# Kernel tuning notes

Hardware: AMD Instinct MI355X
Metric: run time of the kernel (lower is better)

Reference implementation:

```python
import jax, jax.numpy as jnp
import numpy as np

N_KNOTS = 8
LATENT = 16
DEGREE = 3


def _de_boor(x, t, c, p):
    # x: arbitrary-shape query points; t: (n_knots+6,) padded knots; c: (n_knots+2,) control points
    k = jnp.digitize(x, t) - 1  # interval index per element (binary search gather)
    d = [c[k + (j - p)] for j in range(p + 1)]
    for r in range(1, p + 1):
        for j in range(p, r - 1, -1):
            t_lo = t[k + (j - p)]
            t_hi = t[k + (j + 1 - r)]
            alpha = (x - t_lo) / (t_hi - t_lo)
            d[j] = (1.0 - alpha) * d[j - 1] + alpha * d[j]
    return d[p]


def setup_inputs() -> dict:
    key = jax.random.key(0)
    ks = jax.random.split(key, 8)
    # |k| grid normalized to fftfreq range: values in [0, sqrt(3)]
    x = jax.random.uniform(ks[0], (256, 256, 256), dtype=jnp.float32) * 1.7320508
    a = jax.random.uniform(ks[1], (1,), dtype=jnp.float32)  # scale factor in (0,1)
    inv = 1.0 / np.sqrt(LATENT).astype(np.float32)
    W1 = jax.random.normal(ks[2], (1, LATENT), jnp.float32)
    b1 = jnp.zeros((LATENT,), jnp.float32)
    W2 = jax.random.normal(ks[3], (LATENT, LATENT), jnp.float32) * inv
    b2 = jnp.zeros((LATENT,), jnp.float32)
    Ww = jax.random.normal(ks[4], (LATENT, N_KNOTS + 1), jnp.float32) * inv
    bw = jnp.zeros((N_KNOTS + 1,), jnp.float32)
    Wk = jax.random.normal(ks[5], (LATENT, N_KNOTS - 1), jnp.float32) * inv
    bk = jnp.zeros((N_KNOTS - 1,), jnp.float32)
    return {"x": x, "a": a, "W1": W1, "b1": b1, "W2": W2, "b2": b2,
            "Ww": Ww, "bw": bw, "Wk": Wk, "bk": bk}


def reference(x, a, W1, b1, W2, b2, Ww, bw, Wk, bk):
    # tiny MLP on scalar a -> spline weights w and knot increments k
    net = jnp.sin(a @ W1 + b1)           # (LATENT,)
    net = jnp.sin(net @ W2 + b2)         # (LATENT,)
    w = net @ Ww + bw                    # (N_KNOTS+1,)
    kk = net @ Wk + bk                   # (N_KNOTS-1,)
    kk = jnp.concatenate([jnp.zeros((1,), x.dtype), jnp.cumsum(jax.nn.softmax(kk))])  # (N_KNOTS,), monotone in [0,1]
    w = jnp.concatenate([jnp.zeros((1,), x.dtype), w])                                 # (N_KNOTS+2,)
    ak = jnp.concatenate([jnp.zeros((3,), x.dtype), kk, jnp.ones((3,), x.dtype)])      # padded knots
    xq = jnp.clip(x / jnp.sqrt(jnp.asarray(3.0, x.dtype)), 0.0, 1.0 - 0.0001)
    return _de_boor(xq, ak, w, DEGREE)
```

## Files before the change

### kernel.cpp

```cpp
#include <hip/hip_runtime.h>
#include <math.h>

typedef float f4 __attribute__((ext_vector_type(4)));

__device__ __forceinline__ float eval_one(float xv,
                                          float c0, float c1, float c2, float c3,
                                          float k1, float k2, float k3,
                                          float k4, float k5, float k6,
                                          float e1, float e2, float e3,
                                          float e4, float e5, float e6)
{
    const float xq = fminf(fmaxf(xv * 0.57735026918962576f, 0.0f), 0.9999f);
    float acc = fmaf(fmaf(fmaf(c3, xq, c2), xq, c1), xq, c0);
    float r;
    r = fmaxf(xq - k1, 0.f); acc = fmaf(e1 * r, r * r, acc);
    r = fmaxf(xq - k2, 0.f); acc = fmaf(e2 * r, r * r, acc);
    r = fmaxf(xq - k3, 0.f); acc = fmaf(e3 * r, r * r, acc);
    r = fmaxf(xq - k4, 0.f); acc = fmaf(e4 * r, r * r, acc);
    r = fmaxf(xq - k5, 0.f); acc = fmaf(e5 * r, r * r, acc);
    r = fmaxf(xq - k6, 0.f); acc = fmaf(e6 * r, r * r, acc);
    return acc;
}

__global__ __launch_bounds__(256) void nsf_fused_kernel(
    const float* __restrict__ x,
    const float* __restrict__ a,
    const float* __restrict__ W1, const float* __restrict__ b1,
    const float* __restrict__ W2, const float* __restrict__ b2,
    const float* __restrict__ Ww, const float* __restrict__ bw,
    const float* __restrict__ Wk, const float* __restrict__ bk,
    float* __restrict__ out, int n)
{
    const int n4 = n >> 2;
    const int gid = blockIdx.x * blockDim.x + threadIdx.x;
    const int stride = gridDim.x * blockDim.x;
    const f4* __restrict__ x4 = reinterpret_cast<const f4*>(x);
    f4* __restrict__ o4 = reinterpret_cast<f4*>(out);

    f4 v[8];
#pragma unroll
    for (int it = 0; it < 8; ++it) {
        const int idx = gid + it * stride;
        if (idx < n4) v[it] = __builtin_nontemporal_load(x4 + idx);
    }

    const int lane = threadIdx.x & 63;
    const int j16 = lane & 15;

    const float n1own = __sinf(a[0] * W1[j16] + b1[j16]);
    float s2 = b2[j16];
#pragma unroll
    for (int i = 0; i < 16; ++i)
        s2 = fmaf(__shfl(n1own, i, 64), W2[i * 16 + j16], s2);
    const float n2own = __sinf(s2);

    float n2[16];
#pragma unroll
    for (int i = 0; i < 16; ++i) n2[i] = __shfl(n2own, i, 64);

    float w[9];
#pragma unroll
    for (int j = 0; j < 9; ++j) {
        float s = bw[j];
#pragma unroll
        for (int i = 0; i < 16; ++i) s = fmaf(n2[i], Ww[i * 9 + j], s);
        w[j] = s;
    }
    float kr[7];
#pragma unroll
    for (int j = 0; j < 7; ++j) {
        float s = bk[j];
#pragma unroll
        for (int i = 0; i < 16; ++i) s = fmaf(n2[i], Wk[i * 7 + j], s);
        kr[j] = s;
    }

    float m = kr[0];
#pragma unroll
    for (int j = 1; j < 7; ++j) m = fmaxf(m, kr[j]);
    float ee[7], se = 0.f;
#pragma unroll
    for (int j = 0; j < 7; ++j) { ee[j] = __expf(kr[j] - m); se += ee[j]; }
    const float sinv = __builtin_amdgcn_rcpf(se);

    float t[14], cc[10];
    t[0] = t[1] = t[2] = t[3] = 0.f;
    {
        float cum = 0.f;
#pragma unroll
        for (int j = 0; j < 7; ++j) { cum += ee[j] * sinv; t[4 + j] = cum; }
    }
    t[11] = t[12] = t[13] = 1.f;
    cc[0] = 0.f;
#pragma unroll
    for (int j = 0; j < 9; ++j) cc[1 + j] = w[j];

    float p0c0 = 0.f, p0c1 = 0.f, p0c2 = 0.f, p0c3 = 0.f;
    float d3v[7];
#pragma unroll
    for (int iv = 0; iv < 7; ++iv) {
        const int k = 3 + iv;
        const float tk = t[k];
        float d[4][4];
#pragma unroll
        for (int j = 0; j < 4; ++j) {
            d[j][0] = cc[k - 3 + j];
            d[j][1] = d[j][2] = d[j][3] = 0.f;
        }
#pragma unroll
        for (int r = 1; r <= 3; ++r) {
#pragma unroll
            for (int jj = 0; jj < 3; ++jj) {
                const int j = 3 - jj;
                if (j < r) continue;
                const float tlo = t[k + j - 3];
                const float thi = t[k + j + 1 - r];
                const float B = __builtin_amdgcn_rcpf(thi - tlo);
                const float A = (tk - tlo) * B;
                float nd[4];
#pragma unroll
                for (int nn = 0; nn < 4; ++nn) nd[nn] = d[j - 1][nn];
#pragma unroll
                for (int nn = 0; nn < 3; ++nn) {
                    if (nn < r) {
                        const float en = d[j][nn] - d[j - 1][nn];
                        nd[nn]     += A * en;
                        nd[nn + 1] += B * en;
                    }
                }
#pragma unroll
                for (int nn = 0; nn < 4; ++nn) d[j][nn] = nd[nn];
            }
        }
        d3v[iv] = d[3][3];
        if (iv == 0) { p0c0 = d[3][0]; p0c1 = d[3][1]; p0c2 = d[3][2]; p0c3 = d[3][3]; }
    }

    const float k1 = t[4], k2 = t[5], k3 = t[6], k4 = t[7], k5 = t[8], k6 = t[9];
    const float e1 = d3v[1] - d3v[0], e2 = d3v[2] - d3v[1], e3 = d3v[3] - d3v[2];
    const float e4 = d3v[4] - d3v[3], e5 = d3v[5] - d3v[4], e6 = d3v[6] - d3v[5];

#pragma unroll
    for (int it = 0; it < 8; ++it) {
        const int idx = gid + it * stride;
        if (idx < n4) {
            f4 r;
            r.x = eval_one(v[it].x, p0c0,p0c1,p0c2,p0c3, k1,k2,k3,k4,k5,k6, e1,e2,e3,e4,e5,e6);
            r.y = eval_one(v[it].y, p0c0,p0c1,p0c2,p0c3, k1,k2,k3,k4,k5,k6, e1,e2,e3,e4,e5,e6);
            r.z = eval_one(v[it].z, p0c0,p0c1,p0c2,p0c3, k1,k2,k3,k4,k5,k6, e1,e2,e3,e4,e5,e6);
            r.w = eval_one(v[it].w, p0c0,p0c1,p0c2,p0c3, k1,k2,k3,k4,k5,k6, e1,e2,e3,e4,e5,e6);
            __builtin_nontemporal_store(r, o4 + idx);
        }
    }
    for (int idx = gid + 8 * stride; idx < n4; idx += stride) {
        const f4 vv = x4[idx];
        f4 r;
        r.x = eval_one(vv.x, p0c0,p0c1,p0c2,p0c3, k1,k2,k3,k4,k5,k6, e1,e2,e3,e4,e5,e6);
        r.y = eval_one(vv.y, p0c0,p0c1,p0c2,p0c3, k1,k2,k3,k4,k5,k6, e1,e2,e3,e4,e5,e6);
        r.z = eval_one(vv.z, p0c0,p0c1,p0c2,p0c3, k1,k2,k3,k4,k5,k6, e1,e2,e3,e4,e5,e6);
        r.w = eval_one(vv.w, p0c0,p0c1,p0c2,p0c3, k1,k2,k3,k4,k5,k6, e1,e2,e3,e4,e5,e6);
        o4[idx] = r;
    }
    for (int j = (n4 << 2) + gid; j < n; j += stride)
        out[j] = eval_one(x[j], p0c0,p0c1,p0c2,p0c3, k1,k2,k3,k4,k5,k6, e1,e2,e3,e4,e5,e6);
}

extern "C" void kernel_launch(void* const* d_in, const int* in_sizes, int n_in,
                              void* d_out, int out_size, void* d_ws, size_t ws_size,
                              hipStream_t stream)
{
    const float* x  = (const float*)d_in[0];
    const float* a  = (const float*)d_in[1];
    const float* W1 = (const float*)d_in[2];
    const float* b1 = (const float*)d_in[3];
    const float* W2 = (const float*)d_in[4];
    const float* b2 = (const float*)d_in[5];
    const float* Ww = (const float*)d_in[6];
    const float* bw = (const float*)d_in[7];
    const float* Wk = (const float*)d_in[8];
    const float* bk = (const float*)d_in[9];
    float* out = (float*)d_out;
    const int n = out_size;

    const int n4 = n >> 2;
    int blocks = (n4 + 256 * 8 - 1) / (256 * 8);
    if (blocks < 1) blocks = 1;

    hipLaunchKernelGGL(nsf_fused_kernel, dim3(blocks), dim3(256), 0, stream,
                       x, a, W1, b1, W2, b2, Ww, bw, Wk, bk, out, n);
}
```

Measured before the change: 143.4 us.

## Compute spline coefficients via derivative recurrences and lane-parallel MLP head

```diff
diff --git a/kernel.cpp b/kernel.cpp
--- a/kernel.cpp
+++ b/kernel.cpp
@@ -4,14 +4,14 @@
 typedef float f4 __attribute__((ext_vector_type(4)));
 
 __device__ __forceinline__ float eval_one(float xv,
-                                          float c0, float c1, float c2, float c3,
+                                          float c1, float c2, float c3,
                                           float k1, float k2, float k3,
                                           float k4, float k5, float k6,
                                           float e1, float e2, float e3,
                                           float e4, float e5, float e6)
 {
     const float xq = fminf(fmaxf(xv * 0.57735026918962576f, 0.0f), 0.9999f);
-    float acc = fmaf(fmaf(fmaf(c3, xq, c2), xq, c1), xq, c0);
+    float acc = xq * fmaf(fmaf(c3, xq, c2), xq, c1);
     float r;
     r = fmaxf(xq - k1, 0.f); acc = fmaf(e1 * r, r * r, acc);
     r = fmaxf(xq - k2, 0.f); acc = fmaf(e2 * r, r * r, acc);
@@ -22,7 +22,7 @@
     return acc;
 }
 
-__global__ __launch_bounds__(256) void nsf_fused_kernel(
+__global__ __launch_bounds__(256) void nsf_fused2_kernel(
     const float* __restrict__ x,
     const float* __restrict__ a,
     const float* __restrict__ W1, const float* __restrict__ b1,
@@ -37,6 +37,23 @@
     const f4* __restrict__ x4 = reinterpret_cast<const f4*>(x);
     f4* __restrict__ o4 = reinterpret_cast<f4*>(out);
 
+    const int j16 = threadIdx.x & 15;
+
+    const float av  = a[0];
+    const float w1v = W1[j16];
+    const float b1v = b1[j16];
+    const float b2v = b2[j16];
+    float w2l[16];
+#pragma unroll
+    for (int i = 0; i < 16; ++i) w2l[i] = W2[i * 16 + j16];
+    const bool isw = (j16 < 9);
+    const float* hW = isw ? (Ww + j16) : (Wk + (j16 - 9));
+    const int hs = isw ? 9 : 7;
+    const float hbv = isw ? bw[j16] : bk[j16 - 9];
+    float hl[16];
+#pragma unroll
+    for (int i = 0; i < 16; ++i) hl[i] = hW[i * hs];
+
     f4 v[8];
 #pragma unroll
     for (int it = 0; it < 8; ++it) {
@@ -44,125 +61,92 @@
         if (idx < n4) v[it] = __builtin_nontemporal_load(x4 + idx);
     }
 
-    const int lane = threadIdx.x & 63;
-    const int j16 = lane & 15;
-
-    const float n1own = __sinf(a[0] * W1[j16] + b1[j16]);
-    float s2 = b2[j16];
+    const float n1own = __sinf(fmaf(av, w1v, b1v));
+    float s2 = b2v;
 #pragma unroll
     for (int i = 0; i < 16; ++i)
-        s2 = fmaf(__shfl(n1own, i, 64), W2[i * 16 + j16], s2);
+        s2 = fmaf(__shfl(n1own, i, 64), w2l[i], s2);
     const float n2own = __sinf(s2);
 
-    float n2[16];
+    float hsum = hbv;
 #pragma unroll
-    for (int i = 0; i < 16; ++i) n2[i] = __shfl(n2own, i, 64);
+    for (int i = 0; i < 16; ++i)
+        hsum = fmaf(__shfl(n2own, i, 64), hl[i], hsum);
 
-    float w[9];
+    float hv[16];
 #pragma unroll
-    for (int j = 0; j < 9; ++j) {
-        float s = bw[j];
+    for (int i = 0; i < 16; ++i) hv[i] = __shfl(hsum, i, 64);
+
+    float m = hv[9];
 #pragma unroll
-        for (int i = 0; i < 16; ++i) s = fmaf(n2[i], Ww[i * 9 + j], s);
-        w[j] = s;
-    }
-    float kr[7];
+    for (int j = 1; j < 7; ++j) m = fmaxf(m, hv[9 + j]);
+    float ex[7], se = 0.f;
 #pragma unroll
-    for (int j = 0; j < 7; ++j) {
-        float s = bk[j];
-#pragma unroll
-        for (int i = 0; i < 16; ++i) s = fmaf(n2[i], Wk[i * 7 + j], s);
-        kr[j] = s;
-    }
-
-    float m = kr[0];
-#pragma unroll
-    for (int j = 1; j < 7; ++j) m = fmaxf(m, kr[j]);
-    float ee[7], se = 0.f;
-#pragma unroll
-    for (int j = 0; j < 7; ++j) { ee[j] = __expf(kr[j] - m); se += ee[j]; }
+    for (int j = 0; j < 7; ++j) { ex[j] = __expf(hv[9 + j] - m); se += ex[j]; }
     const float sinv = __builtin_amdgcn_rcpf(se);
 
-    float t[14], cc[10];
+    float t[14];
     t[0] = t[1] = t[2] = t[3] = 0.f;
     {
         float cum = 0.f;
 #pragma unroll
-        for (int j = 0; j < 7; ++j) { cum += ee[j] * sinv; t[4 + j] = cum; }
+        for (int j = 0; j < 7; ++j) { cum += ex[j] * sinv; t[4 + j] = cum; }
     }
     t[11] = t[12] = t[13] = 1.f;
+
+    float cc[10];
     cc[0] = 0.f;
 #pragma unroll
-    for (int j = 0; j < 9; ++j) cc[1 + j] = w[j];
+    for (int j = 0; j < 9; ++j) cc[1 + j] = hv[j];
 
-    float p0c0 = 0.f, p0c1 = 0.f, p0c2 = 0.f, p0c3 = 0.f;
-    float d3v[7];
+    float c1v[10];
 #pragma unroll
-    for (int iv = 0; iv < 7; ++iv) {
-        const int k = 3 + iv;
-        const float tk = t[k];
-        float d[4][4];
+    for (int i = 1; i < 10; ++i)
+        c1v[i] = 3.f * (cc[i] - cc[i - 1]) * __builtin_amdgcn_rcpf(t[i + 3] - t[i]);
+    float c2v[10];
 #pragma unroll
-        for (int j = 0; j < 4; ++j) {
-            d[j][0] = cc[k - 3 + j];
-            d[j][1] = d[j][2] = d[j][3] = 0.f;
-        }
+    for (int i = 2; i < 10; ++i)
+        c2v[i] = 2.f * (c1v[i] - c1v[i - 1]) * __builtin_amdgcn_rcpf(t[i + 2] - t[i]);
+    float c3v[10];
 #pragma unroll
-        for (int r = 1; r <= 3; ++r) {
-#pragma unroll
-            for (int jj = 0; jj < 3; ++jj) {
-                const int j = 3 - jj;
-                if (j < r) continue;
-                const float tlo = t[k + j - 3];
-                const float thi = t[k + j + 1 - r];
-                const float B = __builtin_amdgcn_rcpf(thi - tlo);
-                const float A = (tk - tlo) * B;
-                float nd[4];
-#pragma unroll
-                for (int nn = 0; nn < 4; ++nn) nd[nn] = d[j - 1][nn];
-#pragma unroll
-                for (int nn = 0; nn < 3; ++nn) {
-                    if (nn < r) {
-                        const float en = d[j][nn] - d[j - 1][nn];
-                        nd[nn]     += A * en;
-                        nd[nn + 1] += B * en;
-                    }
-                }
-#pragma unroll
-                for (int nn = 0; nn < 4; ++nn) d[j][nn] = nd[nn];
-            }
-        }
-        d3v[iv] = d[3][3];
-        if (iv == 0) { p0c0 = d[3][0]; p0c1 = d[3][1]; p0c2 = d[3][2]; p0c3 = d[3][3]; }
-    }
+    for (int i = 3; i < 10; ++i)
+        c3v[i] = (c2v[i] - c2v[i - 1]) * __builtin_amdgcn_rcpf(t[i + 1] - t[i]);
+
+    const float p0c1 = c1v[1];
+    const float p0c2 = c2v[2] * 0.5f;
+    const float p0c3 = c3v[3] * (1.f / 6.f);
 
     const float k1 = t[4], k2 = t[5], k3 = t[6], k4 = t[7], k5 = t[8], k6 = t[9];
-    const float e1 = d3v[1] - d3v[0], e2 = d3v[2] - d3v[1], e3 = d3v[3] - d3v[2];
-    const float e4 = d3v[4] - d3v[3], e5 = d3v[5] - d3v[4], e6 = d3v[6] - d3v[5];
+    const float e1 = (c3v[4] - c3v[3]) * (1.f / 6.f);
+    const float e2 = (c3v[5] - c3v[4]) * (1.f / 6.f);
+    const float e3 = (c3v[6] - c3v[5]) * (1.f / 6.f);
+    const float e4 = (c3v[7] - c3v[6]) * (1.f / 6.f);
+    const float e5 = (c3v[8] - c3v[7]) * (1.f / 6.f);
+    const float e6 = (c3v[9] - c3v[8]) * (1.f / 6.f);
 
 #pragma unroll
     for (int it = 0; it < 8; ++it) {
         const int idx = gid + it * stride;
         if (idx < n4) {
             f4 r;
-            r.x = eval_one(v[it].x, p0c0,p0c1,p0c2,p0c3, k1,k2,k3,k4,k5,k6, e1,e2,e3,e4,e5,e6);
-            r.y = eval_one(v[it].y, p0c0,p0c1,p0c2,p0c3, k1,k2,k3,k4,k5,k6, e1,e2,e3,e4,e5,e6);
-            r.z = eval_one(v[it].z, p0c0,p0c1,p0c2,p0c3, k1,k2,k3,k4,k5,k6, e1,e2,e3,e4,e5,e6);
-            r.w = eval_one(v[it].w, p0c0,p0c1,p0c2,p0c3, k1,k2,k3,k4,k5,k6, e1,e2,e3,e4,e5,e6);
+            r.x = eval_one(v[it].x, p0c1,p0c2,p0c3, k1,k2,k3,k4,k5,k6, e1,e2,e3,e4,e5,e6);
+            r.y = eval_one(v[it].y, p0c1,p0c2,p0c3, k1,k2,k3,k4,k5,k6, e1,e2,e3,e4,e5,e6);
+            r.z = eval_one(v[it].z, p0c1,p0c2,p0c3, k1,k2,k3,k4,k5,k6, e1,e2,e3,e4,e5,e6);
+            r.w = eval_one(v[it].w, p0c1,p0c2,p0c3, k1,k2,k3,k4,k5,k6, e1,e2,e3,e4,e5,e6);
             __builtin_nontemporal_store(r, o4 + idx);
         }
     }
     for (int idx = gid + 8 * stride; idx < n4; idx += stride) {
         const f4 vv = x4[idx];
         f4 r;
-        r.x = eval_one(vv.x, p0c0,p0c1,p0c2,p0c3, k1,k2,k3,k4,k5,k6, e1,e2,e3,e4,e5,e6);
-        r.y = eval_one(vv.y, p0c0,p0c1,p0c2,p0c3, k1,k2,k3,k4,k5,k6, e1,e2,e3,e4,e5,e6);
-        r.z = eval_one(vv.z, p0c0,p0c1,p0c2,p0c3, k1,k2,k3,k4,k5,k6, e1,e2,e3,e4,e5,e6);
-        r.w = eval_one(vv.w, p0c0,p0c1,p0c2,p0c3, k1,k2,k3,k4,k5,k6, e1,e2,e3,e4,e5,e6);
+        r.x = eval_one(vv.x, p0c1,p0c2,p0c3, k1,k2,k3,k4,k5,k6, e1,e2,e3,e4,e5,e6);
+        r.y = eval_one(vv.y, p0c1,p0c2,p0c3, k1,k2,k3,k4,k5,k6, e1,e2,e3,e4,e5,e6);
+        r.z = eval_one(vv.z, p0c1,p0c2,p0c3, k1,k2,k3,k4,k5,k6, e1,e2,e3,e4,e5,e6);
+        r.w = eval_one(vv.w, p0c1,p0c2,p0c3, k1,k2,k3,k4,k5,k6, e1,e2,e3,e4,e5,e6);
         o4[idx] = r;
     }
     for (int j = (n4 << 2) + gid; j < n; j += stride)
-        out[j] = eval_one(x[j], p0c0,p0c1,p0c2,p0c3, k1,k2,k3,k4,k5,k6, e1,e2,e3,e4,e5,e6);
+        out[j] = eval_one(x[j], p0c1,p0c2,p0c3, k1,k2,k3,k4,k5,k6, e1,e2,e3,e4,e5,e6);
 }
 
 extern "C" void kernel_launch(void* const* d_in, const int* in_sizes, int n_in,
@@ -186,6 +170,6 @@
     int blocks = (n4 + 256 * 8 - 1) / (256 * 8);
     if (blocks < 1) blocks = 1;
 
-    hipLaunchKernelGGL(nsf_fused_kernel, dim3(blocks), dim3(256), 0, stream,
+    hipLaunchKernelGGL(nsf_fused2_kernel, dim3(blocks), dim3(256), 0, stream,
                        x, a, W1, b1, W2, b2, Ww, bw, Wk, bk, out, n);
 }
```

New measurement: 141.2 us. About the same (-1.6%).
